# Kernel optimization log

Hardware: AMD Instinct MI355X
Metric: run time of the kernel (lower is better)

## Reference

```python
import jax, jax.numpy as jnp
import numpy as np

HIDDEN = 1024
HORIZON = 24
BATCH, SEQ, D_IN = 256, 512, 64


def setup_inputs() -> dict:
    key = jax.random.key(0)
    k1, k2, k3, k4, k5 = jax.random.split(key, 5)
    fan_in = D_IN + HIDDEN
    # flax Dense default: lecun_normal kernel, zero bias; use scaled normal
    W = jax.random.normal(k1, (fan_in, 4 * HIDDEN), jnp.float32) / np.sqrt(fan_in)
    b = jnp.zeros((4 * HIDDEN,), jnp.float32)
    Wout = jax.random.normal(k2, (HIDDEN, HORIZON), jnp.float32) / np.sqrt(HIDDEN)
    bout = jnp.zeros((HORIZON,), jnp.float32)
    x = jax.random.normal(k3, (BATCH, SEQ, D_IN), jnp.float32)
    return {"x": x, "W": W, "b": b, "Wout": Wout, "bout": bout}


def reference(x, W, b, Wout, bout):
    B, T, D = x.shape
    H = W.shape[1] // 4

    def step(carry, x_t):
        h, c = carry
        gates = jnp.concatenate([x_t, h], axis=-1) @ W + b  # [B, 4H]
        i, f, g, o = jnp.split(gates, 4, axis=-1)
        i = jax.nn.sigmoid(i)
        f = jax.nn.sigmoid(f)
        o = jax.nn.sigmoid(o)
        g = jnp.tanh(g)
        c = f * c + i * g
        h = o * jnp.tanh(c)
        return (h, c), None

    init = (jnp.zeros((B, H), x.dtype), jnp.zeros((B, H), x.dtype))
    (h_final, _), _ = jax.lax.scan(step, init, jnp.swapaxes(x, 0, 1))
    return h_final @ Wout + bout  # [B, horizon]
```

## Files before the change

kernel.cpp:

```cpp
#include <hip/hip_runtime.h>
#include <hip/hip_fp16.h>


#define T_STEPS 512
#define HID 1024
#define GRID 256
#define NTHR 512

typedef __attribute__((ext_vector_type(8))) _Float16 half8;
typedef __attribute__((ext_vector_type(4))) float f32x4;
typedef __attribute__((ext_vector_type(2))) float f32x2;

__device__ __forceinline__ float sigm(float v) {
    return __builtin_amdgcn_rcpf(1.0f + __expf(-v));
}
__device__ __forceinline__ float tanh_fast(float v) {
    return 2.0f * __builtin_amdgcn_rcpf(1.0f + __expf(-2.0f * v)) - 1.0f;
}

__global__ void pack_w(const float* __restrict__ W, _Float16* __restrict__ Wp) {
    int idx = blockIdx.x * 256 + threadIdx.x;
    const int total = 64 * 136 * 64;
    if (idx >= total) return;
    int col = idx & 63;
    int kb = (idx >> 6) % 136;
    int n = (idx >> 6) / 136;
    int oc = ((col & 3) << 10) + (n << 4) + (col >> 2);
    const float* src = W + (size_t)(kb * 8) * 4096 + oc;
    _Float16* dst = Wp + (size_t)idx * 8;
#pragma unroll
    for (int j = 0; j < 8; j++) dst[j] = (_Float16)src[(size_t)j * 4096];
}

__global__ void __launch_bounds__(NTHR, 2) lstm_persist(
    const float* __restrict__ x,
    const _Float16* __restrict__ Wp,
    const float* __restrict__ bias,
    _Float16* __restrict__ hbuf,
    float* __restrict__ hfinal,
    unsigned int* bar)
{
    __shared__ float P[4 * 64 * 64];
    _Float16* hstage = (_Float16*)P;

    int wg = blockIdx.x;
    int xcd = wg & 7, slot = wg >> 3;
    int n = (xcd << 3) + (slot & 7);
    int m = slot >> 3;
    int B0 = m << 6;

    int tid = threadIdx.x;
    int wave = tid >> 6;
    int lane = tid & 63;
    int l15 = lane & 15, l4 = lane >> 4;
    int bb = tid & 63;
    int u0 = tid >> 6;

    float breg[2][4];
#pragma unroll
    for (int q = 0; q < 2; q++) {
        int u = (u0 << 1) + q;
#pragma unroll
        for (int g = 0; g < 4; g++) breg[q][g] = bias[(g << 10) + (n << 4) + u];
    }

    float cst[2] = {0.f, 0.f};

    const size_t HB = (size_t)128 * 256 * 8;
    const _Float16* WpBase = Wp + (size_t)n * 136 * 64 * 8;

    half8 wfr[4][4];
#pragma unroll
    for (int j = 0; j < 4; j++) {
        int kb = ((2 + wave + 8 * j) << 2) + l4;
        const _Float16* wp = WpBase + ((size_t)kb << 9);
#pragma unroll
        for (int nn = 0; nn < 4; nn++) wfr[j][nn] = *(const half8*)(wp + (((nn << 4) + l15) << 3));
    }

    f32x4 acc[4][4];
#pragma unroll
    for (int i = 0; i < 4; i++)
#pragma unroll
        for (int j = 0; j < 4; j++) acc[i][j] = (f32x4){0.f, 0.f, 0.f, 0.f};

    auto XPREP = [&](int tt) {
        if (wave == 2 || wave == 3) {
            int kb = ((wave - 2) << 2) + l4;
            half8 bx[4];
            const _Float16* wp = WpBase + ((size_t)kb << 9);
#pragma unroll
            for (int nn = 0; nn < 4; nn++) bx[nn] = *(const half8*)(wp + (((nn << 4) + l15) << 3));
#pragma unroll
            for (int mm = 0; mm < 4; mm++) {
                const float* xp = x + ((size_t)(B0 + (mm << 4) + l15) * T_STEPS + tt) * 64 + (kb << 3);
                f32x4 lo = *(const f32x4*)xp;
                f32x4 hi = *(const f32x4*)(xp + 4);
                half8 v;
                v[0] = (_Float16)lo[0]; v[1] = (_Float16)lo[1];
                v[2] = (_Float16)lo[2]; v[3] = (_Float16)lo[3];
                v[4] = (_Float16)hi[0]; v[5] = (_Float16)hi[1];
                v[6] = (_Float16)hi[2]; v[7] = (_Float16)hi[3];
#pragma unroll
                for (int nn = 0; nn < 4; nn++)
                    acc[mm][nn] = __builtin_amdgcn_mfma_f32_16x16x32_f16(v, bx[nn], acc[mm][nn], 0, 0, 0);
            }
        }
    };

    XPREP(0);

    for (int t = 0; t < T_STEPS; t++) {
        const _Float16* cur = hbuf + (size_t)(t & 1) * HB;
        _Float16* nxt = hbuf + (size_t)((t + 1) & 1) * HB;

#pragma unroll
        for (int j = 0; j < 4; j++) {
            int kb = ((2 + wave + 8 * j) << 2) + l4;
            unsigned long long* hp =
                (unsigned long long*)(cur + (((size_t)(kb - 8) << 8) + B0 + l15) * 8);
            half8 ah[4];
#pragma unroll
            for (int mm = 0; mm < 4; mm++) {
                union { unsigned long long u[2]; half8 h; } cv;
                cv.u[0] = __hip_atomic_load(hp + (mm << 5), __ATOMIC_RELAXED, __HIP_MEMORY_SCOPE_AGENT);
                cv.u[1] = __hip_atomic_load(hp + (mm << 5) + 1, __ATOMIC_RELAXED, __HIP_MEMORY_SCOPE_AGENT);
                ah[mm] = cv.h;
            }
#pragma unroll
            for (int mm = 0; mm < 4; mm++)
#pragma unroll
                for (int nn = 0; nn < 4; nn++)
                    acc[mm][nn] = __builtin_amdgcn_mfma_f32_16x16x32_f16(ah[mm], wfr[j][nn],
                                                                         acc[mm][nn], 0, 0, 0);
        }

        if (wave < 4) {
#pragma unroll
            for (int mm = 0; mm < 4; mm++)
#pragma unroll
                for (int nn = 0; nn < 4; nn++) {
                    int c = (nn << 4) + l15;
                    int bblk = (mm << 2) + l4;
                    int word = (((wave << 6) + c) << 6) + (((bblk ^ l15) & 15) << 2);
                    *(f32x4*)&P[word] = acc[mm][nn];
                }
        }
        __syncthreads();
        if (wave >= 4) {
            int pw = wave - 4;
#pragma unroll
            for (int mm = 0; mm < 4; mm++)
#pragma unroll
                for (int nn = 0; nn < 4; nn++) {
                    int c = (nn << 4) + l15;
                    int bblk = (mm << 2) + l4;
                    int word = (((pw << 6) + c) << 6) + (((bblk ^ l15) & 15) << 2);
                    f32x4 v = *(f32x4*)&P[word];
                    v += acc[mm][nn];
                    *(f32x4*)&P[word] = v;
                }
        }
        __syncthreads();

        union { _Float16 h2[2]; unsigned int u; } hs;
        float hvf[2];
#pragma unroll
        for (int q = 0; q < 2; q++) {
            int u = (u0 << 1) + q;
            float g4[4];
#pragma unroll
            for (int g = 0; g < 4; g++) {
                int c = (u << 2) + g;
                int word = (c << 6) + (((((bb >> 2) ^ c) & 15) << 2) | (bb & 3));
                float s = breg[q][g];
#pragma unroll
                for (int w = 0; w < 4; w++) s += P[(w << 12) + word];
                g4[g] = s;
            }
            float ig = sigm(g4[0]);
            float fg = sigm(g4[1]);
            float gg = tanh_fast(g4[2]);
            float og = sigm(g4[3]);
            float cv = fg * cst[q] + ig * gg;
            cst[q] = cv;
            float hv = og * tanh_fast(cv);
            hs.h2[q] = (_Float16)hv;
            hvf[q] = hv;
        }
        if (t == T_STEPS - 1) {
            int ug0 = (n << 4) + (u0 << 1);
            f32x2 hv2; hv2[0] = hvf[0]; hv2[1] = hvf[1];
            *(f32x2*)&hfinal[(size_t)(B0 + bb) * HID + ug0] = hv2;
            break;
        }

        __syncthreads();
        *(unsigned int*)&hstage[(bb << 4) + (u0 << 1)] = hs.u;
        __syncthreads();
        if (tid < 128) {
            int row = tid >> 1, hf = tid & 1;
            union { half8 h; unsigned long long u[2]; } v;
            v.h = *(const half8*)&hstage[(row << 4) + (hf << 3)];
            unsigned long long* dst =
                (unsigned long long*)(nxt + (((size_t)((n << 1) + hf) << 8) + B0 + row) * 8);
            __hip_atomic_store(dst, v.u[0], __ATOMIC_RELAXED, __HIP_MEMORY_SCOPE_AGENT);
            __hip_atomic_store(dst + 1, v.u[1], __ATOMIC_RELAXED, __HIP_MEMORY_SCOPE_AGENT);
        }
        asm volatile("s_waitcnt vmcnt(0)" ::: "memory");
        __syncthreads();

        if (tid == 0)
            __hip_atomic_store(bar + (wg << 4), (unsigned int)(t + 1), __ATOMIC_RELAXED,
                               __HIP_MEMORY_SCOPE_AGENT);
#pragma unroll
        for (int i = 0; i < 4; i++)
#pragma unroll
            for (int j = 0; j < 4; j++) acc[i][j] = (f32x4){0.f, 0.f, 0.f, 0.f};
        XPREP(t + 1);
        if (tid >= 256) {
            const unsigned int* ap = bar + ((tid - 256) << 4);
            while (__hip_atomic_load(ap, __ATOMIC_RELAXED, __HIP_MEMORY_SCOPE_AGENT) <
                   (unsigned int)(t + 1)) {
                __builtin_amdgcn_s_sleep(1);
            }
        }
        __syncthreads();
    }
}

__global__ void proj_kernel(const float* __restrict__ hfinal, const float* __restrict__ Wout,
                            const float* __restrict__ bout, float* __restrict__ out) {
    int b = blockIdx.x;
    int l = threadIdx.x;
    float acc[24];
#pragma unroll
    for (int j = 0; j < 24; j++) acc[j] = 0.f;
    for (int i = 0; i < 16; i++) {
        int k = i * 64 + l;
        float h = hfinal[(size_t)b * HID + k];
        const float* wr = Wout + (size_t)k * 24;
#pragma unroll
        for (int j = 0; j < 24; j++) acc[j] += h * wr[j];
    }
    __shared__ float red[24][65];
#pragma unroll
    for (int j = 0; j < 24; j++) red[j][l] = acc[j];
    __syncthreads();
    if (l < 24) {
        float s = bout[l];
#pragma unroll
        for (int i = 0; i < 64; i++) s += red[l][i];
        out[b * 24 + l] = s;
    }
}

extern "C" void kernel_launch(void* const* d_in, const int* in_sizes, int n_in,
                              void* d_out, int out_size, void* d_ws, size_t ws_size,
                              hipStream_t stream) {
    const float* x = (const float*)d_in[0];
    const float* W = (const float*)d_in[1];
    const float* b = (const float*)d_in[2];
    const float* Wout = (const float*)d_in[3];
    const float* bout = (const float*)d_in[4];
    float* out = (float*)d_out;

    char* ws = (char*)d_ws;
    _Float16* Wp = (_Float16*)ws;
    _Float16* hbuf = (_Float16*)(ws + 8912896);
    float* hfinal = (float*)(ws + 8912896 + 1048576);
    unsigned int* bar = (unsigned int*)(ws + 8912896 + 2097152);

    hipMemsetAsync(hbuf, 0, (size_t)128 * 256 * 8 * sizeof(_Float16), stream);
    hipMemsetAsync(bar, 0, 16384, stream);

    pack_w<<<(64 * 136 * 64 + 255) / 256, 256, 0, stream>>>(W, Wp);

    void* args[6];
    args[0] = (void*)&x;
    args[1] = (void*)&Wp;
    args[2] = (void*)&b;
    args[3] = (void*)&hbuf;
    args[4] = (void*)&hfinal;
    args[5] = (void*)&bar;
    hipLaunchCooperativeKernel((void*)lstm_persist, dim3(GRID), dim3(NTHR), args, 0, stream);

    proj_kernel<<<256, 64, 0, stream>>>(hfinal, Wout, bout, out);
}
```

Before: 3.561 ms.

## Retile LSTM blocks to 32 batch by 128 gate columns with group-local barrier

Measured after the change: 4.426 ms. +24.3%, slower.

```diff
diff --git a/kernel.cpp b/kernel.cpp
--- a/kernel.cpp
+++ b/kernel.cpp
@@ -20,12 +20,12 @@
 
 __global__ void pack_w(const float* __restrict__ W, _Float16* __restrict__ Wp) {
     int idx = blockIdx.x * 256 + threadIdx.x;
-    const int total = 64 * 136 * 64;
+    const int total = 32 * 136 * 128;
     if (idx >= total) return;
-    int col = idx & 63;
-    int kb = (idx >> 6) % 136;
-    int n = (idx >> 6) / 136;
-    int oc = ((col & 3) << 10) + (n << 4) + (col >> 2);
+    int col = idx & 127;
+    int kb = (idx >> 7) % 136;
+    int ng = (idx >> 7) / 136;
+    int oc = ((col & 3) << 10) + (ng << 5) + (col >> 2);
     const float* src = W + (size_t)(kb * 8) * 4096 + oc;
     _Float16* dst = Wp + (size_t)idx * 8;
 #pragma unroll
@@ -40,70 +40,81 @@
     float* __restrict__ hfinal,
     unsigned int* bar)
 {
-    __shared__ float P[4 * 64 * 64];
+    __shared__ float P[4 * 128 * 32];
     _Float16* hstage = (_Float16*)P;
 
     int wg = blockIdx.x;
-    int xcd = wg & 7, slot = wg >> 3;
-    int n = (xcd << 3) + (slot & 7);
-    int m = slot >> 3;
-    int B0 = m << 6;
+    int mg = wg >> 5;
+    int ng = wg & 31;
+    int B0 = mg << 5;
 
     int tid = threadIdx.x;
     int wave = tid >> 6;
     int lane = tid & 63;
     int l15 = lane & 15, l4 = lane >> 4;
-    int bb = tid & 63;
-    int u0 = tid >> 6;
+    int bb = tid & 31;
+    int us = tid >> 5;
 
     float breg[2][4];
 #pragma unroll
     for (int q = 0; q < 2; q++) {
-        int u = (u0 << 1) + q;
-#pragma unroll
-        for (int g = 0; g < 4; g++) breg[q][g] = bias[(g << 10) + (n << 4) + u];
+        int u = (us << 1) + q;
+#pragma unroll
+        for (int g = 0; g < 4; g++) breg[q][g] = bias[(g << 10) + (ng << 5) + u];
     }
 
     float cst[2] = {0.f, 0.f};
 
     const size_t HB = (size_t)128 * 256 * 8;
-    const _Float16* WpBase = Wp + (size_t)n * 136 * 64 * 8;
-
-    half8 wfr[4][4];
+    const _Float16* WpBase = Wp + (size_t)ng * 136 * 1024;
+
+    half8 wfr[4][8];
 #pragma unroll
     for (int j = 0; j < 4; j++) {
         int kb = ((2 + wave + 8 * j) << 2) + l4;
-        const _Float16* wp = WpBase + ((size_t)kb << 9);
-#pragma unroll
-        for (int nn = 0; nn < 4; nn++) wfr[j][nn] = *(const half8*)(wp + (((nn << 4) + l15) << 3));
-    }
-
-    f32x4 acc[4][4];
-#pragma unroll
-    for (int i = 0; i < 4; i++)
-#pragma unroll
-        for (int j = 0; j < 4; j++) acc[i][j] = (f32x4){0.f, 0.f, 0.f, 0.f};
+        const _Float16* wp = WpBase + ((size_t)kb << 10);
+#pragma unroll
+        for (int nn = 0; nn < 8; nn++) wfr[j][nn] = *(const half8*)(wp + (((nn << 4) + l15) << 3));
+    }
+
+    f32x4 acc[2][8];
+#pragma unroll
+    for (int i = 0; i < 2; i++)
+#pragma unroll
+        for (int j = 0; j < 8; j++) acc[i][j] = (f32x4){0.f, 0.f, 0.f, 0.f};
 
     auto XPREP = [&](int tt) {
         if (wave == 2 || wave == 3) {
             int kb = ((wave - 2) << 2) + l4;
-            half8 bx[4];
-            const _Float16* wp = WpBase + ((size_t)kb << 9);
-#pragma unroll
-            for (int nn = 0; nn < 4; nn++) bx[nn] = *(const half8*)(wp + (((nn << 4) + l15) << 3));
-#pragma unroll
-            for (int mm = 0; mm < 4; mm++) {
+            half8 v[2];
+#pragma unroll
+            for (int mm = 0; mm < 2; mm++) {
                 const float* xp = x + ((size_t)(B0 + (mm << 4) + l15) * T_STEPS + tt) * 64 + (kb << 3);
                 f32x4 lo = *(const f32x4*)xp;
                 f32x4 hi = *(const f32x4*)(xp + 4);
-                half8 v;
-                v[0] = (_Float16)lo[0]; v[1] = (_Float16)lo[1];
-                v[2] = (_Float16)lo[2]; v[3] = (_Float16)lo[3];
-                v[4] = (_Float16)hi[0]; v[5] = (_Float16)hi[1];
-                v[6] = (_Float16)hi[2]; v[7] = (_Float16)hi[3];
-#pragma unroll
-                for (int nn = 0; nn < 4; nn++)
-                    acc[mm][nn] = __builtin_amdgcn_mfma_f32_16x16x32_f16(v, bx[nn], acc[mm][nn], 0, 0, 0);
+                half8 t;
+                t[0] = (_Float16)lo[0]; t[1] = (_Float16)lo[1];
+                t[2] = (_Float16)lo[2]; t[3] = (_Float16)lo[3];
+                t[4] = (_Float16)hi[0]; t[5] = (_Float16)hi[1];
+                t[6] = (_Float16)hi[2]; t[7] = (_Float16)hi[3];
+                v[mm] = t;
+            }
+            const _Float16* wp = WpBase + ((size_t)kb << 10);
+#pragma unroll
+            for (int h2 = 0; h2 < 2; h2++) {
+                half8 bx[4];
+#pragma unroll
+                for (int i = 0; i < 4; i++) {
+                    int nn = (h2 << 2) + i;
+                    bx[i] = *(const half8*)(wp + (((nn << 4) + l15) << 3));
+                }
+#pragma unroll
+                for (int mm = 0; mm < 2; mm++)
+#pragma unroll
+                    for (int i = 0; i < 4; i++)
+                        acc[mm][(h2 << 2) + i] =
+                            __builtin_amdgcn_mfma_f32_16x16x32_f16(v[mm], bx[i],
+                                                                   acc[mm][(h2 << 2) + i], 0, 0, 0);
             }
         }
     };
@@ -119,46 +130,47 @@
             int kb = ((2 + wave + 8 * j) << 2) + l4;
             unsigned long long* hp =
                 (unsigned long long*)(cur + (((size_t)(kb - 8) << 8) + B0 + l15) * 8);
-            half8 ah[4];
-#pragma unroll
-            for (int mm = 0; mm < 4; mm++) {
+            half8 ah[2];
+#pragma unroll
+            for (int mm = 0; mm < 2; mm++) {
                 union { unsigned long long u[2]; half8 h; } cv;
                 cv.u[0] = __hip_atomic_load(hp + (mm << 5), __ATOMIC_RELAXED, __HIP_MEMORY_SCOPE_AGENT);
                 cv.u[1] = __hip_atomic_load(hp + (mm << 5) + 1, __ATOMIC_RELAXED, __HIP_MEMORY_SCOPE_AGENT);
                 ah[mm] = cv.h;
             }
 #pragma unroll
-            for (int mm = 0; mm < 4; mm++)
-#pragma unroll
-                for (int nn = 0; nn < 4; nn++)
+            for (int mm = 0; mm < 2; mm++)
+#pragma unroll
+                for (int nn = 0; nn < 8; nn++)
                     acc[mm][nn] = __builtin_amdgcn_mfma_f32_16x16x32_f16(ah[mm], wfr[j][nn],
                                                                          acc[mm][nn], 0, 0, 0);
         }
 
         if (wave < 4) {
-#pragma unroll
-            for (int mm = 0; mm < 4; mm++)
-#pragma unroll
-                for (int nn = 0; nn < 4; nn++) {
+            float* Pq = P + (wave << 12);
+#pragma unroll
+            for (int mm = 0; mm < 2; mm++)
+#pragma unroll
+                for (int nn = 0; nn < 8; nn++) {
                     int c = (nn << 4) + l15;
                     int bblk = (mm << 2) + l4;
-                    int word = (((wave << 6) + c) << 6) + (((bblk ^ l15) & 15) << 2);
-                    *(f32x4*)&P[word] = acc[mm][nn];
+                    int word = (c << 5) + (((bblk ^ l15) & 7) << 2);
+                    *(f32x4*)&Pq[word] = acc[mm][nn];
                 }
         }
         __syncthreads();
         if (wave >= 4) {
-            int pw = wave - 4;
-#pragma unroll
-            for (int mm = 0; mm < 4; mm++)
-#pragma unroll
-                for (int nn = 0; nn < 4; nn++) {
+            float* Pq = P + ((wave - 4) << 12);
+#pragma unroll
+            for (int mm = 0; mm < 2; mm++)
+#pragma unroll
+                for (int nn = 0; nn < 8; nn++) {
                     int c = (nn << 4) + l15;
                     int bblk = (mm << 2) + l4;
-                    int word = (((pw << 6) + c) << 6) + (((bblk ^ l15) & 15) << 2);
-                    f32x4 v = *(f32x4*)&P[word];
+                    int word = (c << 5) + (((bblk ^ l15) & 7) << 2);
+                    f32x4 v = *(f32x4*)&Pq[word];
                     v += acc[mm][nn];
-                    *(f32x4*)&P[word] = v;
+                    *(f32x4*)&Pq[word] = v;
                 }
         }
         __syncthreads();
@@ -167,12 +179,12 @@
         float hvf[2];
 #pragma unroll
         for (int q = 0; q < 2; q++) {
-            int u = (u0 << 1) + q;
+            int u = (us << 1) + q;
             float g4[4];
 #pragma unroll
             for (int g = 0; g < 4; g++) {
                 int c = (u << 2) + g;
-                int word = (c << 6) + (((((bb >> 2) ^ c) & 15) << 2) | (bb & 3));
+                int word = (c << 5) + (((((bb >> 2) ^ c) & 7) << 2) | (bb & 3));
                 float s = breg[q][g];
 #pragma unroll
                 for (int w = 0; w < 4; w++) s += P[(w << 12) + word];
@@ -189,21 +201,21 @@
             hvf[q] = hv;
         }
         if (t == T_STEPS - 1) {
-            int ug0 = (n << 4) + (u0 << 1);
+            int ug0 = (ng << 5) + (us << 1);
             f32x2 hv2; hv2[0] = hvf[0]; hv2[1] = hvf[1];
             *(f32x2*)&hfinal[(size_t)(B0 + bb) * HID + ug0] = hv2;
             break;
         }
 
         __syncthreads();
-        *(unsigned int*)&hstage[(bb << 4) + (u0 << 1)] = hs.u;
+        *(unsigned int*)&hstage[(bb << 5) + (us << 1)] = hs.u;
         __syncthreads();
         if (tid < 128) {
-            int row = tid >> 1, hf = tid & 1;
+            int row = tid >> 2, q = tid & 3;
             union { half8 h; unsigned long long u[2]; } v;
-            v.h = *(const half8*)&hstage[(row << 4) + (hf << 3)];
+            v.h = *(const half8*)&hstage[(row << 5) + (q << 3)];
             unsigned long long* dst =
-                (unsigned long long*)(nxt + (((size_t)((n << 1) + hf) << 8) + B0 + row) * 8);
+                (unsigned long long*)(nxt + (((size_t)((ng << 2) + q) << 8) + B0 + row) * 8);
             __hip_atomic_store(dst, v.u[0], __ATOMIC_RELAXED, __HIP_MEMORY_SCOPE_AGENT);
             __hip_atomic_store(dst + 1, v.u[1], __ATOMIC_RELAXED, __HIP_MEMORY_SCOPE_AGENT);
         }
@@ -214,12 +226,12 @@
             __hip_atomic_store(bar + (wg << 4), (unsigned int)(t + 1), __ATOMIC_RELAXED,
                                __HIP_MEMORY_SCOPE_AGENT);
 #pragma unroll
-        for (int i = 0; i < 4; i++)
-#pragma unroll
-            for (int j = 0; j < 4; j++) acc[i][j] = (f32x4){0.f, 0.f, 0.f, 0.f};
+        for (int i = 0; i < 2; i++)
+#pragma unroll
+            for (int j = 0; j < 8; j++) acc[i][j] = (f32x4){0.f, 0.f, 0.f, 0.f};
         XPREP(t + 1);
-        if (tid >= 256) {
-            const unsigned int* ap = bar + ((tid - 256) << 4);
+        if (tid >= 256 && tid < 288) {
+            const unsigned int* ap = bar + (((mg << 5) + (tid - 256)) << 4);
             while (__hip_atomic_load(ap, __ATOMIC_RELAXED, __HIP_MEMORY_SCOPE_AGENT) <
                    (unsigned int)(t + 1)) {
                 __builtin_amdgcn_s_sleep(1);
@@ -274,7 +286,7 @@
     hipMemsetAsync(hbuf, 0, (size_t)128 * 256 * 8 * sizeof(_Float16), stream);
     hipMemsetAsync(bar, 0, 16384, stream);
 
-    pack_w<<<(64 * 136 * 64 + 255) / 256, 256, 0, stream>>>(W, Wp);
+    pack_w<<<(32 * 136 * 128 + 255) / 256, 256, 0, stream>>>(W, Wp);
 
     void* args[6];
     args[0] = (void*)&x;
```
